# Optimization experiments

Measured on AMD Instinct MI355X. Metric: run time of the kernel, lower is better.

## Reference

```python
import jax, jax.numpy as jnp
import numpy as np

NUM_HEADS = 4
WORD_DIM = 100
LEAKY_ALPHA = 0.3  # keras LeakyReLU default negative_slope


def setup_inputs() -> dict:
    key = jax.random.key(0)
    k1, k2, k3 = jax.random.split(key, 3)
    x = jax.random.normal(k1, (8, 30, 20, 40, WORD_DIM), dtype=jnp.float32)
    # keras 'random_normal' initializer: stddev 0.05
    w_att = jax.random.normal(k2, (NUM_HEADS, WORD_DIM), dtype=jnp.float32) * 0.05
    b_att = jax.random.normal(k3, (NUM_HEADS, WORD_DIM), dtype=jnp.float32) * 0.05
    return {"x": x, "w_att": w_att, "b_att": b_att}


def reference(x, w_att, b_att):
    # x: [B, T, E, W, D]; w_att, b_att: [H, D]
    B, T, E, W, D = x.shape
    H = w_att.shape[0]
    type_emb = x[..., 0, :]        # [B,T,E,D]
    words = x[..., 1:, :]          # [B,T,E,N,D], N = W-1
    # per-head hidden representation: leaky_relu(w*words + b)
    pre = words[..., None, :, :] * w_att[:, None, :] + b_att[:, None, :]  # [B,T,E,H,N,D]
    hidden = jnp.where(pre >= 0, pre, LEAKY_ALPHA * pre)
    # attention scores: dot(type_emb, hidden) over D
    scores = jnp.einsum('bted,btehnd->btehn', type_emb, hidden)  # [B,T,E,H,N]
    # original uses raw exp / sum (no max-subtraction) -- keep faithful
    att = jnp.exp(scores)
    att = att / jnp.sum(att, axis=-1, keepdims=True)
    out = jnp.einsum('btehn,btend->bthed'.replace('bthed', 'btehd'), att, words)  # [B,T,E,H,D]
    out = out.reshape(B, T, E, H * D)
    # all-zero events map to zero embeddings
    nonzero = jnp.any(x != 0, axis=(-1, -2), keepdims=False)  # [B,T,E]
    out = jnp.where(nonzero[..., None], out, 0.0)
    return out
```

## Files before the change

### kernel.cpp

```cpp
#include <hip/hip_runtime.h>
#include <math.h>
#include <stdint.h>

#define NHEAD 4
#define DD 100
#define NW 39
#define BLOCK 256

typedef float v2f __attribute__((ext_vector_type(2)));
typedef __attribute__((address_space(3))) uint32_t lds_t;
typedef const __attribute__((address_space(1))) uint32_t glb_t;

__global__ __launch_bounds__(BLOCK, 6) void ts_enc(
    const float* __restrict__ x,
    const float* __restrict__ w_att,
    const float* __restrict__ b_att,
    float* __restrict__ out)
{
    __shared__ float tile[40 * DD];
    __shared__ float scp[NHEAD][4][40];

    const int tid  = threadIdx.x;
    const int wv   = __builtin_amdgcn_readfirstlane(tid >> 6);
    const int lane = tid & 63;
    const float* xsite = x + (size_t)blockIdx.x * (40 * DD);

    #pragma unroll
    for (int i = 0; i < 4; ++i) {
        const int cf = i * BLOCK + tid;
        if (cf < 1000) {
            glb_t* g = (glb_t*)(xsite + cf * 4);
            lds_t* l = (lds_t*)(tile + (i * BLOCK + wv * 64) * 4);
            __builtin_amdgcn_global_load_lds(g, l, 16, 0, 0);
        }
    }
    __syncthreads();

    const bool act  = lane < NW;
    const int  nrow = act ? lane : NW - 1;
    const float* wrow = tile + (1 + nrow) * DD;

    v2f accA[NHEAD] = {{0,0},{0,0},{0,0},{0,0}};
    v2f accB[NHEAD] = {{0,0},{0,0},{0,0},{0,0}};

#define ABODY(cc) { \
        const int c_ = (cc); \
        const v2f x01 = *(const v2f*)(wrow + c_ * 4); \
        const v2f x23 = *(const v2f*)(wrow + c_ * 4 + 2); \
        const v2f t01 = *(const v2f*)(tile + c_ * 4); \
        const v2f t23 = *(const v2f*)(tile + c_ * 4 + 2); \
        _Pragma("unroll") \
        for (int h = 0; h < NHEAD; ++h) { \
            const v2f w01 = *(const v2f*)(w_att + h * DD + c_ * 4); \
            const v2f w23 = *(const v2f*)(w_att + h * DD + c_ * 4 + 2); \
            const v2f b01 = *(const v2f*)(b_att + h * DD + c_ * 4); \
            const v2f b23 = *(const v2f*)(b_att + h * DD + c_ * 4 + 2); \
            const v2f p01 = x01 * w01 + b01; \
            const v2f p23 = x23 * w23 + b23; \
            const v2f l01 = __builtin_elementwise_max(p01, 0.3f * p01); \
            const v2f l23 = __builtin_elementwise_max(p23, 0.3f * p23); \
            accA[h] = t01 * l01 + accA[h]; \
            accB[h] = t23 * l23 + accB[h]; \
        } }

    #pragma unroll
    for (int j = 0; j < 6; ++j) ABODY(wv * 6 + j)
    if (wv == 0) ABODY(24)
#undef ABODY

    if (act) {
        #pragma unroll
        for (int h = 0; h < NHEAD; ++h)
            scp[h][wv][lane] = (accA[h].x + accA[h].y) + (accB[h].x + accB[h].y);
    }
    __syncthreads();

    float sc = 0.f;
    if (act) sc = (scp[wv][0][lane] + scp[wv][1][lane])
                + (scp[wv][2][lane] + scp[wv][3][lane]);
    const float e = act ? __expf(sc) : 0.f;
    float sm = e;
    #pragma unroll
    for (int off = 32; off; off >>= 1) sm += __shfl_xor(sm, off);
    const float att = e / sm;

    const int l2 = lane < 50 ? lane : 49;
    const float* wb = tile + DD + l2 * 2;
    float ox = 0.f, oy = 0.f;
    #pragma unroll
    for (int n = 0; n < NW; ++n) {
        const float attn = __builtin_bit_cast(float,
            __builtin_amdgcn_readlane(__builtin_bit_cast(int, att), n));
        const v2f wd = *(const v2f*)(wb + n * DD);
        ox = fmaf(attn, wd.x, ox);
        oy = fmaf(attn, wd.y, oy);
    }
    if (lane < 50) {
        const v2f o = {ox, oy};
        *(v2f*)(out + (size_t)blockIdx.x * (NHEAD * DD) + wv * DD + lane * 2) = o;
    }
}

extern "C" void kernel_launch(void* const* d_in, const int* in_sizes, int n_in,
                              void* d_out, int out_size, void* d_ws, size_t ws_size,
                              hipStream_t stream) {
    const float* x     = (const float*)d_in[0];
    const float* w_att = (const float*)d_in[1];
    const float* b_att = (const float*)d_in[2];
    float* out = (float*)d_out;

    const int sites = 8 * 30 * 20;
    ts_enc<<<sites, BLOCK, 0, stream>>>(x, w_att, b_att, out);
}
```

Measured before the change: 27.50 us.

## Batch weight loads as float4, read type row from global, defer softmax normalization

Raises the launch-bounds occupancy hint from 6 to 8 waves. The score loop now loads w_att and b_att as float4 in batches of three chunks for two heads at a time, and reads the type-embedding row directly from global memory instead of LDS. The softmax wave-shuffle reduction is removed: the sum of exponentials is accumulated inside the output loop and applied as a single reciprocal multiply at the end. These changes aim to cut shuffle latency and load instruction count, at the cost of extra global loads and tighter register budgets under the higher occupancy target.

```diff
diff --git a/kernel.cpp b/kernel.cpp
--- a/kernel.cpp
+++ b/kernel.cpp
@@ -11,7 +11,7 @@
 typedef __attribute__((address_space(3))) uint32_t lds_t;
 typedef const __attribute__((address_space(1))) uint32_t glb_t;
 
-__global__ __launch_bounds__(BLOCK, 6) void ts_enc(
+__global__ __launch_bounds__(BLOCK, 8) void ts_enc(
     const float* __restrict__ x,
     const float* __restrict__ w_att,
     const float* __restrict__ b_att,
@@ -43,30 +43,55 @@
     v2f accA[NHEAD] = {{0,0},{0,0},{0,0},{0,0}};
     v2f accB[NHEAD] = {{0,0},{0,0},{0,0},{0,0}};
 
-#define ABODY(cc) { \
-        const int c_ = (cc); \
-        const v2f x01 = *(const v2f*)(wrow + c_ * 4); \
-        const v2f x23 = *(const v2f*)(wrow + c_ * 4 + 2); \
-        const v2f t01 = *(const v2f*)(tile + c_ * 4); \
-        const v2f t23 = *(const v2f*)(tile + c_ * 4 + 2); \
-        _Pragma("unroll") \
-        for (int h = 0; h < NHEAD; ++h) { \
-            const v2f w01 = *(const v2f*)(w_att + h * DD + c_ * 4); \
-            const v2f w23 = *(const v2f*)(w_att + h * DD + c_ * 4 + 2); \
-            const v2f b01 = *(const v2f*)(b_att + h * DD + c_ * 4); \
-            const v2f b23 = *(const v2f*)(b_att + h * DD + c_ * 4 + 2); \
-            const v2f p01 = x01 * w01 + b01; \
-            const v2f p23 = x23 * w23 + b23; \
-            const v2f l01 = __builtin_elementwise_max(p01, 0.3f * p01); \
-            const v2f l23 = __builtin_elementwise_max(p23, 0.3f * p23); \
-            accA[h] = t01 * l01 + accA[h]; \
-            accB[h] = t23 * l23 + accB[h]; \
-        } }
+#define CBODY(c_, h_, w4, b4) { \
+        const v2f w01 = {w4.x, w4.y}, w23 = {w4.z, w4.w}; \
+        const v2f b01 = {b4.x, b4.y}, b23 = {b4.z, b4.w}; \
+        const v2f p01 = x01 * w01 + b01; \
+        const v2f p23 = x23 * w23 + b23; \
+        const v2f l01 = __builtin_elementwise_max(p01, 0.3f * p01); \
+        const v2f l23 = __builtin_elementwise_max(p23, 0.3f * p23); \
+        accA[h_] = t01 * l01 + accA[h_]; \
+        accB[h_] = t23 * l23 + accB[h_]; }
 
     #pragma unroll
-    for (int j = 0; j < 6; ++j) ABODY(wv * 6 + j)
-    if (wv == 0) ABODY(24)
-#undef ABODY
+    for (int hp = 0; hp < 2; ++hp) {
+        #pragma unroll
+        for (int jh = 0; jh < 2; ++jh) {
+            float4 ws0[3], ws1[3], bs0[3], bs1[3];
+            #pragma unroll
+            for (int j = 0; j < 3; ++j) {
+                const int c_ = wv * 6 + jh * 3 + j;
+                ws0[j] = *(const float4*)(w_att + (2 * hp    ) * DD + c_ * 4);
+                ws1[j] = *(const float4*)(w_att + (2 * hp + 1) * DD + c_ * 4);
+                bs0[j] = *(const float4*)(b_att + (2 * hp    ) * DD + c_ * 4);
+                bs1[j] = *(const float4*)(b_att + (2 * hp + 1) * DD + c_ * 4);
+            }
+            #pragma unroll
+            for (int j = 0; j < 3; ++j) {
+                const int c_ = wv * 6 + jh * 3 + j;
+                const v2f x01 = *(const v2f*)(wrow + c_ * 4);
+                const v2f x23 = *(const v2f*)(wrow + c_ * 4 + 2);
+                const v2f t01 = *(const v2f*)(xsite + c_ * 4);
+                const v2f t23 = *(const v2f*)(xsite + c_ * 4 + 2);
+                CBODY(c_, 2 * hp,     ws0[j], bs0[j])
+                CBODY(c_, 2 * hp + 1, ws1[j], bs1[j])
+            }
+        }
+    }
+    if (wv == 0) {
+        const int c_ = 24;
+        const v2f x01 = *(const v2f*)(wrow + c_ * 4);
+        const v2f x23 = *(const v2f*)(wrow + c_ * 4 + 2);
+        const v2f t01 = *(const v2f*)(xsite + c_ * 4);
+        const v2f t23 = *(const v2f*)(xsite + c_ * 4 + 2);
+        #pragma unroll
+        for (int h = 0; h < NHEAD; ++h) {
+            const float4 w4 = *(const float4*)(w_att + h * DD + c_ * 4);
+            const float4 b4 = *(const float4*)(b_att + h * DD + c_ * 4);
+            CBODY(c_, h, w4, b4)
+        }
+    }
+#undef CBODY
 
     if (act) {
         #pragma unroll
@@ -79,25 +104,23 @@
     if (act) sc = (scp[wv][0][lane] + scp[wv][1][lane])
                 + (scp[wv][2][lane] + scp[wv][3][lane]);
     const float e = act ? __expf(sc) : 0.f;
-    float sm = e;
-    #pragma unroll
-    for (int off = 32; off; off >>= 1) sm += __shfl_xor(sm, off);
-    const float att = e / sm;
 
     const int l2 = lane < 50 ? lane : 49;
     const float* wb = tile + DD + l2 * 2;
-    float ox = 0.f, oy = 0.f;
+    v2f o = {0.f, 0.f};
+    float s = 0.f;
     #pragma unroll
     for (int n = 0; n < NW; ++n) {
-        const float attn = __builtin_bit_cast(float,
-            __builtin_amdgcn_readlane(__builtin_bit_cast(int, att), n));
+        const float en = __builtin_bit_cast(float,
+            __builtin_amdgcn_readlane(__builtin_bit_cast(int, e), n));
         const v2f wd = *(const v2f*)(wb + n * DD);
-        ox = fmaf(attn, wd.x, ox);
-        oy = fmaf(attn, wd.y, oy);
+        o = en * wd + o;
+        s += en;
     }
+    const float r = 1.f / s;
     if (lane < 50) {
-        const v2f o = {ox, oy};
-        *(v2f*)(out + (size_t)blockIdx.x * (NHEAD * DD) + wv * DD + lane * 2) = o;
+        const v2f q = o * r;
+        *(v2f*)(out + (size_t)blockIdx.x * (NHEAD * DD) + wv * DD + lane * 2) = q;
     }
 }
 
```

Result: slower. 51.41 us (+86.9%).
